# Kernel tuning notes

Hardware: AMD Instinct MI355X
Metric: run time of the kernel (lower is better)

The kernel has to match this reference:

```python
import jax, jax.numpy as jnp
import numpy as np

B, J, D, K = 2048, 15, 9, 20
HID, NF = 256, 24


def _linear_params(key, fin, fout):
    kw, kb = jax.random.split(key)
    lim = 1.0 / np.sqrt(fin)
    W = jax.random.uniform(kw, (fin, fout), minval=-lim, maxval=lim, dtype=jnp.float32)
    b = jax.random.uniform(kb, (fout,), minval=-lim, maxval=lim, dtype=jnp.float32)
    return W, b


def setup_inputs() -> dict:
    key = jax.random.key(0)
    ks = jax.random.split(key, 9)
    inp = {"dct_input": jax.random.normal(ks[0], (B, J, D, K), dtype=jnp.float32)}
    inp["q_W1"], inp["q_b1"] = _linear_params(ks[1], K, HID)
    inp["q_W2"], inp["q_b2"] = _linear_params(ks[2], HID, HID)
    inp["k_W1"], inp["k_b1"] = _linear_params(ks[3], K, HID)
    inp["k_W2"], inp["k_b2"] = _linear_params(ks[4], HID, HID)
    inp["v_W1"], inp["v_b1"] = _linear_params(ks[5], K, HID)
    inp["v_W2"], inp["v_b2"] = _linear_params(ks[6], HID, HID)
    inp["p_W1"], inp["p_b1"] = _linear_params(ks[7], 2 * HID, HID)
    inp["p_W2"], inp["p_b2"] = _linear_params(ks[8], HID, NF)
    return inp


def _mlp(x, W1, b1, W2, b2):
    return jax.nn.relu(x @ W1 + b1) @ W2 + b2


def _idct_basis(n):
    # IDCT of DCT-II with norm='ortho' (scipy.fftpack.idct default type=2):
    # x[t] = sum_k c_k * X[k] * cos(pi*k*(2t+1)/(2n)), c_0=sqrt(1/n), c_k=sqrt(2/n)
    k = jnp.arange(n, dtype=jnp.float32)[:, None]
    t = jnp.arange(n, dtype=jnp.float32)[None, :]
    c = jnp.full((n, 1), np.sqrt(2.0 / n), dtype=jnp.float32).at[0, 0].set(np.sqrt(1.0 / n))
    return c * jnp.cos(np.pi * k * (2.0 * t + 1.0) / (2.0 * n))  # [k, t]


def reference(dct_input, q_W1, q_b1, q_W2, q_b2, k_W1, k_b1, k_W2, k_b2,
              v_W1, v_b1, v_W2, v_b2, p_W1, p_b1, p_W2, p_b2):
    b, j, d, kdim = dct_input.shape
    x = dct_input.reshape(b, j * d, kdim)          # tokens = J*D
    Q = _mlp(x, q_W1, q_b1, q_W2, q_b2)            # [B, T, H]
    Kt = _mlp(x, k_W1, k_b1, k_W2, k_b2)
    V = _mlp(x, v_W1, v_b1, v_W2, v_b2)
    scores = jnp.einsum('bth,bsh->bts', Q, Kt) / np.sqrt(Q.shape[-1])
    attn = jax.nn.softmax(scores, axis=-1)
    context = jnp.einsum('bts,bsh->bth', attn, V)
    feat = jnp.concatenate([Q, context], axis=-1)  # [B, T, 2H]
    out = _mlp(feat, p_W1, p_b1, p_W2, p_b2)       # [B, T, NF] (DCT coeffs)
    out = out.reshape(b, j, d, NF).transpose(0, 3, 1, 2)  # [B, NF, J, D]
    M = _idct_basis(NF)                            # [NF(k), NF(t)]
    time = jnp.einsum('bkjd,kt->btjd', out, M)     # inverse DCT along time axis
    pred = time.reshape(b, NF, j, 3, 3)
    return pred
```

## Files before the change

### kernel.cpp

```cpp
#include <hip/hip_runtime.h>

#define BDIM 512

typedef float f32x4 __attribute__((ext_vector_type(4)));
typedef short bf16x8 __attribute__((ext_vector_type(8)));

#define MFMA(a, b, c) __builtin_amdgcn_mfma_f32_16x16x32_bf16((a), (b), (c), 0, 0, 0)

constexpr int OQ1 = 0;
constexpr int OK1w = 8192;
constexpr int OV1 = 16384;
constexpr int OQ2 = 24576;
constexpr int OK2w = 90112;
constexpr int OV2 = 155648;
constexpr int OP1 = 221184;
constexpr int OP2 = 352256;
constexpr int WTOT = 360448;

constexpr int OFF_Q   = 0;
constexpr int OFF_XS  = 73728;
constexpr int OFF_SP  = 83968;
constexpr int OFF_HT2 = 127776;
constexpr int OFF_KVT = 144160;
constexpr int OFF_RWL = 160544;
constexpr int SMEM_BYTES = 161120;

constexpr int SPS = 152;

__device__ __forceinline__ unsigned short f2b(float f) {
  unsigned int u = __float_as_uint(f);
  return (unsigned short)((u + 0x7fffu + ((u >> 16) & 1u)) >> 16);
}
__device__ __forceinline__ float bfu(unsigned short u) {
  return __uint_as_float(((unsigned int)u) << 16);
}

__device__ __forceinline__ bf16x8 frag(const unsigned short* m, int rb, int stride,
                                       int kb, int lane) {
  return *(const bf16x8*)(m + (rb + (lane & 15)) * stride + kb + ((lane >> 4) << 3));
}
__device__ __forceinline__ bf16x8 frag256s(const unsigned short* m, int rb, int kb, int lane) {
  const int row = rb + (lane & 15);
  const int c = (kb + ((lane >> 4) << 3)) ^ ((row & 7) << 3);
  return *(const bf16x8*)(m + row * 256 + c);
}
__device__ __forceinline__ bf16x8 frag32s(const unsigned short* m, int rb, int lane) {
  const int row = rb + (lane & 15);
  const int c = ((lane >> 4) << 3) ^ (((row >> 1) & 3) << 3);
  return *(const bf16x8*)(m + row * 32 + c);
}
__device__ __forceinline__ int swz256(int r, int c) { return r * 256 + (c ^ ((r & 7) << 3)); }
__device__ __forceinline__ int swz32 (int r, int c) { return r * 32  + (c ^ (((r >> 1) & 3) << 3)); }

__global__ void prep_w(const float* __restrict__ qW1, const float* __restrict__ qW2,
                       const float* __restrict__ kW1, const float* __restrict__ kW2,
                       const float* __restrict__ vW1, const float* __restrict__ vW2,
                       const float* __restrict__ pW1, const float* __restrict__ pW2,
                       unsigned short* __restrict__ ws) {
  int i = blockIdx.x * 256 + threadIdx.x;
  if (i >= WTOT) return;
  float v = 0.f;
  if (i < OQ2) {
    int sel = i >> 13, r = i & 8191;
    int o = r >> 5, k = r & 31;
    const float* W = (sel == 0) ? qW1 : (sel == 1) ? kW1 : vW1;
    if (k < 20) v = W[k * 256 + o];
  } else if (i < OP1) {
    int r = i - OQ2;
    int sel = r >> 16, q = r & 65535;
    int o = q >> 8, k = q & 255;
    const float* W = (sel == 0) ? qW2 : (sel == 1) ? kW2 : vW2;
    v = W[k * 256 + o];
  } else if (i < OP2) {
    int r = i - OP1;
    int o = r >> 9, f = r & 511;
    v = pW1[f * 256 + o];
  } else {
    int r = i - OP2;
    int o = r >> 8, k = r & 255;
    if (o < 24) v = pW2[k * 24 + o];
  }
  ws[i] = f2b(v);
}

__global__ __launch_bounds__(BDIM, 2)
void motion_mfma(const float* __restrict__ x,
                 const float* __restrict__ qb1v, const float* __restrict__ qb2v,
                 const float* __restrict__ kb1v, const float* __restrict__ kb2v,
                 const float* __restrict__ vb1v, const float* __restrict__ vb2v,
                 const float* __restrict__ pb1v, const float* __restrict__ pb2v,
                 const unsigned short* __restrict__ ws,
                 float* __restrict__ out) {
  extern __shared__ char smem[];
  unsigned short* Qs  = (unsigned short*)(smem + OFF_Q);
  unsigned short* XS  = (unsigned short*)(smem + OFF_XS);
  unsigned short* SP  = (unsigned short*)(smem + OFF_SP);
  unsigned short* Hc  = (unsigned short*)(smem + OFF_SP);
  unsigned short* HT2 = (unsigned short*)(smem + OFF_HT2);
  unsigned short* KVT = (unsigned short*)(smem + OFF_KVT);
  float* RWL = (float*)(smem + OFF_RWL);
  float* Ob  = (float*)(smem + 0);
  float* MT  = (float*)(smem + 14400);

  const int tid = threadIdx.x, lane = tid & 63, w = tid >> 6;
  const int l15 = lane & 15, rs = ((lane >> 4) << 2);
  const int cb = w * 32;
  const int b = blockIdx.x;
  const f32x4 zf4 = {0.f, 0.f, 0.f, 0.f};
  const bf16x8 zb8 = {0, 0, 0, 0, 0, 0, 0, 0};

  const float* xb = x + (size_t)b * 2700;
  for (int i = tid; i < 160 * 32; i += BDIM) {
    int r = i >> 5, c = i & 31;
    XS[swz32(r, c)] = (r < 135 && c < 20) ? f2b(xb[r * 20 + c]) : (unsigned short)0;
  }
  __syncthreads();

  {
    bf16x8 w0 = frag(ws + OQ1, cb, 32, 0, lane);
    bf16x8 w1 = frag(ws + OQ1, cb + 16, 32, 0, lane);
    float bb0 = qb1v[cb + l15], bb1 = qb1v[cb + 16 + l15];
#pragma unroll
    for (int m = 0; m < 9; ++m) {
      bf16x8 a = frag32s(XS, m * 16, lane);
      f32x4 c0 = MFMA(a, w0, zf4);
      f32x4 c1 = MFMA(a, w1, zf4);
#pragma unroll
      for (int r = 0; r < 4; ++r) {
        Hc[swz256(m * 16 + rs + r, cb + l15)]      = f2b(fmaxf(c0[r] + bb0, 0.f));
        Hc[swz256(m * 16 + rs + r, cb + 16 + l15)] = f2b(fmaxf(c1[r] + bb1, 0.f));
      }
    }
    __syncthreads();

    f32x4 acc[9][2];
#pragma unroll
    for (int m = 0; m < 9; ++m) { acc[m][0] = zf4; acc[m][1] = zf4; }
    for (int ks = 0; ks < 8; ++ks) {
      bf16x8 g0 = frag(ws + OQ2, cb, 256, ks * 32, lane);
      bf16x8 g1 = frag(ws + OQ2, cb + 16, 256, ks * 32, lane);
#pragma unroll
      for (int m = 0; m < 9; ++m) {
        bf16x8 a = frag256s(Hc, m * 16, ks * 32, lane);
        acc[m][0] = MFMA(a, g0, acc[m][0]);
        acc[m][1] = MFMA(a, g1, acc[m][1]);
      }
    }
    float bb20 = qb2v[cb + l15], bb21 = qb2v[cb + 16 + l15];
#pragma unroll
    for (int m = 0; m < 9; ++m)
#pragma unroll
      for (int r = 0; r < 4; ++r) {
        Qs[swz256(m * 16 + rs + r, cb + l15)]      = f2b(acc[m][0][r] + bb20);
        Qs[swz256(m * 16 + rs + r, cb + 16 + l15)] = f2b(acc[m][1][r] + bb21);
      }
  }
  __syncthreads();

  for (int ch = 0; ch < 5; ++ch) {
    const int s0 = ch * 32;
    {
      bf16x8 w0 = frag(ws + OK1w, cb, 32, 0, lane);
      bf16x8 w1 = frag(ws + OK1w, cb + 16, 32, 0, lane);
      float bb0 = kb1v[cb + l15], bb1 = kb1v[cb + 16 + l15];
#pragma unroll
      for (int mm = 0; mm < 2; ++mm) {
        bf16x8 a = frag32s(XS, s0 + mm * 16, lane);
        f32x4 c0 = MFMA(a, w0, zf4), c1 = MFMA(a, w1, zf4);
#pragma unroll
        for (int r = 0; r < 4; ++r) {
          HT2[swz256(mm * 16 + rs + r, cb + l15)]      = f2b(fmaxf(c0[r] + bb0, 0.f));
          HT2[swz256(mm * 16 + rs + r, cb + 16 + l15)] = f2b(fmaxf(c1[r] + bb1, 0.f));
        }
      }
    }
    __syncthreads();
    {
      f32x4 a2[2][2] = {{zf4, zf4}, {zf4, zf4}};
      for (int ks = 0; ks < 8; ++ks) {
        bf16x8 g0 = frag(ws + OK2w, cb, 256, ks * 32, lane);
        bf16x8 g1 = frag(ws + OK2w, cb + 16, 256, ks * 32, lane);
#pragma unroll
        for (int mm = 0; mm < 2; ++mm) {
          bf16x8 a = frag256s(HT2, mm * 16, ks * 32, lane);
          a2[mm][0] = MFMA(a, g0, a2[mm][0]);
          a2[mm][1] = MFMA(a, g1, a2[mm][1]);
        }
      }
      float bb0 = kb2v[cb + l15], bb1 = kb2v[cb + 16 + l15];
#pragma unroll
      for (int mm = 0; mm < 2; ++mm)
#pragma unroll
        for (int r = 0; r < 4; ++r) {
          KVT[swz256(mm * 16 + rs + r, cb + l15)]      = f2b(a2[mm][0][r] + bb0);
          KVT[swz256(mm * 16 + rs + r, cb + 16 + l15)] = f2b(a2[mm][1][r] + bb1);
        }
    }
    __syncthreads();
#pragma unroll
    for (int rep = 0; rep < 3; ++rep) {
      int j = w + rep * 8;
      if (j < 18) {
        int m = j >> 1, n = j & 1;
        int sb = s0 + n * 16;
        if (sb < 144) {
          f32x4 sa = zf4;
          for (int ks = 0; ks < 8; ++ks) {
            bf16x8 qa = frag256s(Qs, m * 16, ks * 32, lane);
            bf16x8 kf = frag256s(KVT, n * 16, ks * 32, lane);
            sa = MFMA(qa, kf, sa);
          }
#pragma unroll
          for (int r = 0; r < 4; ++r)
            SP[(m * 16 + rs + r) * SPS + sb + l15] = f2b(sa[r] * 0.0625f);
        }
      }
    }
    __syncthreads();
  }

#pragma unroll
  for (int pass = 0; pass < 2; ++pass) {
    int r = pass * 128 + (tid >> 2);
    if (r < 144) {
      int j = tid & 3;
      float mx = -1e30f;
      for (int s = j; s < 135; s += 4) mx = fmaxf(mx, bfu(SP[r * SPS + s]));
      mx = fmaxf(mx, __shfl_xor(mx, 1));
      mx = fmaxf(mx, __shfl_xor(mx, 2));
      float sum = 0.f;
      for (int s = j; s < 135; s += 4) {
        float p = __expf(bfu(SP[r * SPS + s]) - mx);
        SP[r * SPS + s] = f2b(p);
        sum += p;
      }
      sum += __shfl_xor(sum, 1);
      sum += __shfl_xor(sum, 2);
      if (j == 0) RWL[r] = sum;
      for (int s = 135 + j; s < 144; s += 4) SP[r * SPS + s] = 0;
    }
  }
  __syncthreads();

  f32x4 ctx[9][2];
#pragma unroll
  for (int m = 0; m < 9; ++m) { ctx[m][0] = zf4; ctx[m][1] = zf4; }
  for (int ch = 0; ch < 5; ++ch) {
    const int s0 = ch * 32;
    {
      bf16x8 w0 = frag(ws + OV1, cb, 32, 0, lane);
      bf16x8 w1 = frag(ws + OV1, cb + 16, 32, 0, lane);
      float bb0 = vb1v[cb + l15], bb1 = vb1v[cb + 16 + l15];
#pragma unroll
      for (int mm = 0; mm < 2; ++mm) {
        bf16x8 a = frag32s(XS, s0 + mm * 16, lane);
        f32x4 c0 = MFMA(a, w0, zf4), c1 = MFMA(a, w1, zf4);
#pragma unroll
        for (int r = 0; r < 4; ++r) {
          HT2[swz256(mm * 16 + rs + r, cb + l15)]      = f2b(fmaxf(c0[r] + bb0, 0.f));
          HT2[swz256(mm * 16 + rs + r, cb + 16 + l15)] = f2b(fmaxf(c1[r] + bb1, 0.f));
        }
      }
    }
    __syncthreads();
    {
      f32x4 a2[2][2] = {{zf4, zf4}, {zf4, zf4}};
      for (int ks = 0; ks < 8; ++ks) {
        bf16x8 g0 = frag(ws + OV2, cb, 256, ks * 32, lane);
        bf16x8 g1 = frag(ws + OV2, cb + 16, 256, ks * 32, lane);
#pragma unroll
        for (int mm = 0; mm < 2; ++mm) {
          bf16x8 a = frag256s(HT2, mm * 16, ks * 32, lane);
          a2[mm][0] = MFMA(a, g0, a2[mm][0]);
          a2[mm][1] = MFMA(a, g1, a2[mm][1]);
        }
      }
      float bb0 = vb2v[cb + l15], bb1 = vb2v[cb + 16 + l15];
#pragma unroll
      for (int mm = 0; mm < 2; ++mm)
#pragma unroll
        for (int r = 0; r < 4; ++r) {
          KVT[swz32(cb + l15,      mm * 16 + rs + r)] = f2b(a2[mm][0][r] + bb0);
          KVT[swz32(cb + 16 + l15, mm * 16 + rs + r)] = f2b(a2[mm][1][r] + bb1);
        }
    }
    __syncthreads();
    {
      bf16x8 v0 = frag32s(KVT, cb, lane);
      bf16x8 v1 = frag32s(KVT, cb + 16, lane);
      const bool mask = (ch == 4) && (lane >= 32);
#pragma unroll
      for (int m = 0; m < 9; ++m) {
        bf16x8 pa = frag(SP, m * 16, SPS, s0, lane);
        if (mask) pa = zb8;
        ctx[m][0] = MFMA(pa, v0, ctx[m][0]);
        ctx[m][1] = MFMA(pa, v1, ctx[m][1]);
      }
    }
  }
  __syncthreads();

#pragma unroll
  for (int m = 0; m < 9; ++m)
#pragma unroll
    for (int r = 0; r < 4; ++r) {
      int t = m * 16 + rs + r;
      float inv = 1.0f / RWL[t];
      Hc[swz256(t, cb + l15)]      = f2b(ctx[m][0][r] * inv);
      Hc[swz256(t, cb + 16 + l15)] = f2b(ctx[m][1][r] * inv);
    }
  __syncthreads();

  {
    float pbias0 = pb1v[cb + l15], pbias1 = pb1v[cb + 16 + l15];
    f32x4 pacc[9][2];
#pragma unroll
    for (int m = 0; m < 9; ++m) {
      pacc[m][0] = (f32x4){pbias0, pbias0, pbias0, pbias0};
      pacc[m][1] = (f32x4){pbias1, pbias1, pbias1, pbias1};
    }
    for (int ks = 0; ks < 16; ++ks) {
      bf16x8 g0 = frag(ws + OP1, cb, 512, ks * 32, lane);
      bf16x8 g1 = frag(ws + OP1, cb + 16, 512, ks * 32, lane);
      const unsigned short* As = (ks < 8) ? Qs : Hc;
      int kk = (ks & 7) * 32;
#pragma unroll
      for (int m = 0; m < 9; ++m) {
        bf16x8 a = frag256s(As, m * 16, kk, lane);
        pacc[m][0] = MFMA(a, g0, pacc[m][0]);
        pacc[m][1] = MFMA(a, g1, pacc[m][1]);
      }
    }
    __syncthreads();
#pragma unroll
    for (int m = 0; m < 9; ++m)
#pragma unroll
      for (int r = 0; r < 4; ++r) {
        Hc[swz256(m * 16 + rs + r, cb + l15)]      = f2b(fmaxf(pacc[m][0][r], 0.f));
        Hc[swz256(m * 16 + rs + r, cb + 16 + l15)] = f2b(fmaxf(pacc[m][1][r], 0.f));
      }
  }
  for (int i = tid; i < 576; i += BDIM) {
    int kk = i / 24, t = i - kk * 24;
    float c = (kk == 0) ? 0.20412414523193150f : 0.28867513459481287f;
    MT[i] = c * cosf(0.065449846949787352f * (float)(kk * (2 * t + 1)));
  }
  __syncthreads();

#pragma unroll
  for (int rep = 0; rep < 3; ++rep) {
    int j = w + rep * 8;
    if (j < 18) {
      int m = j >> 1, n = j & 1;
      f32x4 oa = zf4;
      for (int ks = 0; ks < 8; ++ks) {
        bf16x8 a = frag256s(Hc, m * 16, ks * 32, lane);
        bf16x8 g = frag(ws + OP2, n * 16, 256, ks * 32, lane);
        oa = MFMA(a, g, oa);
      }
      int c = n * 16 + l15;
      if (c < 24) {
        float bb = pb2v[c];
#pragma unroll
        for (int r = 0; r < 4; ++r)
          Ob[(m * 16 + rs + r) * 25 + c] = oa[r] + bb;
      }
    }
  }
  __syncthreads();

  for (int i = tid; i < 3240; i += BDIM) {
    int tt = i / 135, tok = i - tt * 135;
    float a = 0.f;
#pragma unroll
    for (int k = 0; k < 24; ++k)
      a = fmaf(Ob[tok * 25 + k], MT[k * 24 + tt], a);
    out[(size_t)b * 3240 + i] = a;
  }
}

extern "C" void kernel_launch(void* const* d_in, const int* in_sizes, int n_in,
                              void* d_out, int out_size, void* d_ws, size_t ws_size,
                              hipStream_t stream) {
  (void)in_sizes; (void)n_in; (void)out_size;
  if (ws_size < (size_t)WTOT * 2) return;

  const float* x   = (const float*)d_in[0];
  const float* qW1 = (const float*)d_in[1];
  const float* qb1 = (const float*)d_in[2];
  const float* qW2 = (const float*)d_in[3];
  const float* qb2 = (const float*)d_in[4];
  const float* kW1 = (const float*)d_in[5];
  const float* kb1 = (const float*)d_in[6];
  const float* kW2 = (const float*)d_in[7];
  const float* kb2 = (const float*)d_in[8];
  const float* vW1 = (const float*)d_in[9];
  const float* vb1 = (const float*)d_in[10];
  const float* vW2 = (const float*)d_in[11];
  const float* vb2 = (const float*)d_in[12];
  const float* pW1 = (const float*)d_in[13];
  const float* pb1 = (const float*)d_in[14];
  const float* pW2 = (const float*)d_in[15];
  const float* pb2 = (const float*)d_in[16];
  float* out = (float*)d_out;
  unsigned short* ws = (unsigned short*)d_ws;

  prep_w<<<dim3((WTOT + 255) / 256), dim3(256), 0, stream>>>(
      qW1, qW2, kW1, kW2, vW1, vW2, pW1, pW2, ws);

  (void)hipFuncSetAttribute((const void*)motion_mfma,
                            hipFuncAttributeMaxDynamicSharedMemorySize, SMEM_BYTES);
  motion_mfma<<<dim3(2048), dim3(BDIM), SMEM_BYTES, stream>>>(
      x, qb1, qb2, kb1, kb2, vb1, vb2, pb1, pb2, ws, out);
}
```

Baseline: 603.2 us.

## Double block size to 16 waves with one 16-column tile per wave

Raises the workgroup from 512 to 1024 threads, with each wave owning one 16-column output tile instead of two 32-column tiles. Per-wave accumulator arrays shrink by half, which lowers register pressure and aims for more waves in flight to hide MFMA and LDS latency. The softmax now runs in a single pass, and the attention-score and output-projection loops are remapped over 16 waves. Input loads and output stores are switched to nontemporal hints. The launch-bounds hint of 4 blocks of 1024 threads per CU is unlikely to be reachable given the large shared-memory footprint, and the larger block adds barrier cost.

```diff
diff --git a/kernel.cpp b/kernel.cpp
--- a/kernel.cpp
+++ b/kernel.cpp
@@ -1,6 +1,6 @@
 #include <hip/hip_runtime.h>
 
-#define BDIM 512
+#define BDIM 1024
 
 typedef float f32x4 __attribute__((ext_vector_type(4)));
 typedef short bf16x8 __attribute__((ext_vector_type(8)));
@@ -83,7 +83,7 @@
   ws[i] = f2b(v);
 }
 
-__global__ __launch_bounds__(BDIM, 2)
+__global__ __launch_bounds__(BDIM, 4)
 void motion_mfma(const float* __restrict__ x,
                  const float* __restrict__ qb1v, const float* __restrict__ qb2v,
                  const float* __restrict__ kb1v, const float* __restrict__ kb2v,
@@ -104,7 +104,7 @@
 
   const int tid = threadIdx.x, lane = tid & 63, w = tid >> 6;
   const int l15 = lane & 15, rs = ((lane >> 4) << 2);
-  const int cb = w * 32;
+  const int cb = w * 16;
   const int b = blockIdx.x;
   const f32x4 zf4 = {0.f, 0.f, 0.f, 0.f};
   const bf16x8 zb8 = {0, 0, 0, 0, 0, 0, 0, 0};
@@ -112,48 +112,41 @@
   const float* xb = x + (size_t)b * 2700;
   for (int i = tid; i < 160 * 32; i += BDIM) {
     int r = i >> 5, c = i & 31;
-    XS[swz32(r, c)] = (r < 135 && c < 20) ? f2b(xb[r * 20 + c]) : (unsigned short)0;
+    float v = (r < 135 && c < 20) ? __builtin_nontemporal_load(xb + r * 20 + c) : 0.f;
+    XS[swz32(r, c)] = f2b(v);
   }
   __syncthreads();
 
   {
     bf16x8 w0 = frag(ws + OQ1, cb, 32, 0, lane);
-    bf16x8 w1 = frag(ws + OQ1, cb + 16, 32, 0, lane);
-    float bb0 = qb1v[cb + l15], bb1 = qb1v[cb + 16 + l15];
+    float bb0 = qb1v[cb + l15];
 #pragma unroll
     for (int m = 0; m < 9; ++m) {
       bf16x8 a = frag32s(XS, m * 16, lane);
       f32x4 c0 = MFMA(a, w0, zf4);
-      f32x4 c1 = MFMA(a, w1, zf4);
-#pragma unroll
-      for (int r = 0; r < 4; ++r) {
-        Hc[swz256(m * 16 + rs + r, cb + l15)]      = f2b(fmaxf(c0[r] + bb0, 0.f));
-        Hc[swz256(m * 16 + rs + r, cb + 16 + l15)] = f2b(fmaxf(c1[r] + bb1, 0.f));
-      }
-    }
-    __syncthreads();
-
-    f32x4 acc[9][2];
-#pragma unroll
-    for (int m = 0; m < 9; ++m) { acc[m][0] = zf4; acc[m][1] = zf4; }
+#pragma unroll
+      for (int r = 0; r < 4; ++r)
+        Hc[swz256(m * 16 + rs + r, cb + l15)] = f2b(fmaxf(c0[r] + bb0, 0.f));
+    }
+    __syncthreads();
+
+    f32x4 acc[9];
+#pragma unroll
+    for (int m = 0; m < 9; ++m) acc[m] = zf4;
     for (int ks = 0; ks < 8; ++ks) {
       bf16x8 g0 = frag(ws + OQ2, cb, 256, ks * 32, lane);
-      bf16x8 g1 = frag(ws + OQ2, cb + 16, 256, ks * 32, lane);
 #pragma unroll
       for (int m = 0; m < 9; ++m) {
         bf16x8 a = frag256s(Hc, m * 16, ks * 32, lane);
-        acc[m][0] = MFMA(a, g0, acc[m][0]);
-        acc[m][1] = MFMA(a, g1, acc[m][1]);
-      }
-    }
-    float bb20 = qb2v[cb + l15], bb21 = qb2v[cb + 16 + l15];
+        acc[m] = MFMA(a, g0, acc[m]);
+      }
+    }
+    float bb20 = qb2v[cb + l15];
 #pragma unroll
     for (int m = 0; m < 9; ++m)
 #pragma unroll
-      for (int r = 0; r < 4; ++r) {
-        Qs[swz256(m * 16 + rs + r, cb + l15)]      = f2b(acc[m][0][r] + bb20);
-        Qs[swz256(m * 16 + rs + r, cb + 16 + l15)] = f2b(acc[m][1][r] + bb21);
-      }
+      for (int r = 0; r < 4; ++r)
+        Qs[swz256(m * 16 + rs + r, cb + l15)] = f2b(acc[m][r] + bb20);
   }
   __syncthreads();
 
@@ -161,67 +154,57 @@
     const int s0 = ch * 32;
     {
       bf16x8 w0 = frag(ws + OK1w, cb, 32, 0, lane);
-      bf16x8 w1 = frag(ws + OK1w, cb + 16, 32, 0, lane);
-      float bb0 = kb1v[cb + l15], bb1 = kb1v[cb + 16 + l15];
+      float bb0 = kb1v[cb + l15];
 #pragma unroll
       for (int mm = 0; mm < 2; ++mm) {
         bf16x8 a = frag32s(XS, s0 + mm * 16, lane);
-        f32x4 c0 = MFMA(a, w0, zf4), c1 = MFMA(a, w1, zf4);
-#pragma unroll
-        for (int r = 0; r < 4; ++r) {
-          HT2[swz256(mm * 16 + rs + r, cb + l15)]      = f2b(fmaxf(c0[r] + bb0, 0.f));
-          HT2[swz256(mm * 16 + rs + r, cb + 16 + l15)] = f2b(fmaxf(c1[r] + bb1, 0.f));
-        }
-      }
-    }
-    __syncthreads();
-    {
-      f32x4 a2[2][2] = {{zf4, zf4}, {zf4, zf4}};
+        f32x4 c0 = MFMA(a, w0, zf4);
+#pragma unroll
+        for (int r = 0; r < 4; ++r)
+          HT2[swz256(mm * 16 + rs + r, cb + l15)] = f2b(fmaxf(c0[r] + bb0, 0.f));
+      }
+    }
+    __syncthreads();
+    {
+      f32x4 a2[2] = {zf4, zf4};
       for (int ks = 0; ks < 8; ++ks) {
         bf16x8 g0 = frag(ws + OK2w, cb, 256, ks * 32, lane);
-        bf16x8 g1 = frag(ws + OK2w, cb + 16, 256, ks * 32, lane);
 #pragma unroll
         for (int mm = 0; mm < 2; ++mm) {
           bf16x8 a = frag256s(HT2, mm * 16, ks * 32, lane);
-          a2[mm][0] = MFMA(a, g0, a2[mm][0]);
-          a2[mm][1] = MFMA(a, g1, a2[mm][1]);
+          a2[mm] = MFMA(a, g0, a2[mm]);
         }
       }
-      float bb0 = kb2v[cb + l15], bb1 = kb2v[cb + 16 + l15];
+      float bb0 = kb2v[cb + l15];
 #pragma unroll
       for (int mm = 0; mm < 2; ++mm)
 #pragma unroll
-        for (int r = 0; r < 4; ++r) {
-          KVT[swz256(mm * 16 + rs + r, cb + l15)]      = f2b(a2[mm][0][r] + bb0);
-          KVT[swz256(mm * 16 + rs + r, cb + 16 + l15)] = f2b(a2[mm][1][r] + bb1);
-        }
-    }
-    __syncthreads();
-#pragma unroll
-    for (int rep = 0; rep < 3; ++rep) {
-      int j = w + rep * 8;
+        for (int r = 0; r < 4; ++r)
+          KVT[swz256(mm * 16 + rs + r, cb + l15)] = f2b(a2[mm][r] + bb0);
+    }
+    __syncthreads();
+#pragma unroll
+    for (int rep = 0; rep < 2; ++rep) {
+      int j = w + rep * 16;
       if (j < 18) {
         int m = j >> 1, n = j & 1;
         int sb = s0 + n * 16;
-        if (sb < 144) {
-          f32x4 sa = zf4;
-          for (int ks = 0; ks < 8; ++ks) {
-            bf16x8 qa = frag256s(Qs, m * 16, ks * 32, lane);
-            bf16x8 kf = frag256s(KVT, n * 16, ks * 32, lane);
-            sa = MFMA(qa, kf, sa);
-          }
-#pragma unroll
-          for (int r = 0; r < 4; ++r)
-            SP[(m * 16 + rs + r) * SPS + sb + l15] = f2b(sa[r] * 0.0625f);
+        f32x4 sa = zf4;
+        for (int ks = 0; ks < 8; ++ks) {
+          bf16x8 qa = frag256s(Qs, m * 16, ks * 32, lane);
+          bf16x8 kf = frag256s(KVT, n * 16, ks * 32, lane);
+          sa = MFMA(qa, kf, sa);
         }
-      }
-    }
-    __syncthreads();
-  }
-
-#pragma unroll
-  for (int pass = 0; pass < 2; ++pass) {
-    int r = pass * 128 + (tid >> 2);
+#pragma unroll
+        for (int r = 0; r < 4; ++r)
+          SP[(m * 16 + rs + r) * SPS + sb + l15] = f2b(sa[r] * 0.0625f);
+      }
+    }
+    __syncthreads();
+  }
+
+  {
+    int r = tid >> 2;
     if (r < 144) {
       int j = tid & 3;
       float mx = -1e30f;
@@ -242,59 +225,50 @@
   }
   __syncthreads();
 
-  f32x4 ctx[9][2];
-#pragma unroll
-  for (int m = 0; m < 9; ++m) { ctx[m][0] = zf4; ctx[m][1] = zf4; }
+  f32x4 ctx[9];
+#pragma unroll
+  for (int m = 0; m < 9; ++m) ctx[m] = zf4;
   for (int ch = 0; ch < 5; ++ch) {
     const int s0 = ch * 32;
     {
       bf16x8 w0 = frag(ws + OV1, cb, 32, 0, lane);
-      bf16x8 w1 = frag(ws + OV1, cb + 16, 32, 0, lane);
-      float bb0 = vb1v[cb + l15], bb1 = vb1v[cb + 16 + l15];
+      float bb0 = vb1v[cb + l15];
 #pragma unroll
       for (int mm = 0; mm < 2; ++mm) {
         bf16x8 a = frag32s(XS, s0 + mm * 16, lane);
-        f32x4 c0 = MFMA(a, w0, zf4), c1 = MFMA(a, w1, zf4);
-#pragma unroll
-        for (int r = 0; r < 4; ++r) {
-          HT2[swz256(mm * 16 + rs + r, cb + l15)]      = f2b(fmaxf(c0[r] + bb0, 0.f));
-          HT2[swz256(mm * 16 + rs + r, cb + 16 + l15)] = f2b(fmaxf(c1[r] + bb1, 0.f));
-        }
-      }
-    }
-    __syncthreads();
-    {
-      f32x4 a2[2][2] = {{zf4, zf4}, {zf4, zf4}};
+        f32x4 c0 = MFMA(a, w0, zf4);
+#pragma unroll
+        for (int r = 0; r < 4; ++r)
+          HT2[swz256(mm * 16 + rs + r, cb + l15)] = f2b(fmaxf(c0[r] + bb0, 0.f));
+      }
+    }
+    __syncthreads();
+    {
+      f32x4 a2[2] = {zf4, zf4};
       for (int ks = 0; ks < 8; ++ks) {
         bf16x8 g0 = frag(ws + OV2, cb, 256, ks * 32, lane);
-        bf16x8 g1 = frag(ws + OV2, cb + 16, 256, ks * 32, lane);
 #pragma unroll
         for (int mm = 0; mm < 2; ++mm) {
           bf16x8 a = frag256s(HT2, mm * 16, ks * 32, lane);
-          a2[mm][0] = MFMA(a, g0, a2[mm][0]);
-          a2[mm][1] = MFMA(a, g1, a2[mm][1]);
+          a2[mm] = MFMA(a, g0, a2[mm]);
         }
       }
-      float bb0 = vb2v[cb + l15], bb1 = vb2v[cb + 16 + l15];
+      float bb0 = vb2v[cb + l15];
 #pragma unroll
       for (int mm = 0; mm < 2; ++mm)
 #pragma unroll
-        for (int r = 0; r < 4; ++r) {
-          KVT[swz32(cb + l15,      mm * 16 + rs + r)] = f2b(a2[mm][0][r] + bb0);
-          KVT[swz32(cb + 16 + l15, mm * 16 + rs + r)] = f2b(a2[mm][1][r] + bb1);
-        }
+        for (int r = 0; r < 4; ++r)
+          KVT[swz32(cb + l15, mm * 16 + rs + r)] = f2b(a2[mm][r] + bb0);
     }
     __syncthreads();
     {
       bf16x8 v0 = frag32s(KVT, cb, lane);
-      bf16x8 v1 = frag32s(KVT, cb + 16, lane);
       const bool mask = (ch == 4) && (lane >= 32);
 #pragma unroll
       for (int m = 0; m < 9; ++m) {
         bf16x8 pa = frag(SP, m * 16, SPS, s0, lane);
         if (mask) pa = zb8;
-        ctx[m][0] = MFMA(pa, v0, ctx[m][0]);
-        ctx[m][1] = MFMA(pa, v1, ctx[m][1]);
+        ctx[m] = MFMA(pa, v0, ctx[m]);
       }
     }
   }
@@ -306,39 +280,37 @@
     for (int r = 0; r < 4; ++r) {
       int t = m * 16 + rs + r;
       float inv = 1.0f / RWL[t];
-      Hc[swz256(t, cb + l15)]      = f2b(ctx[m][0][r] * inv);
-      Hc[swz256(t, cb + 16 + l15)] = f2b(ctx[m][1][r] * inv);
+      Hc[swz256(t, cb + l15)] = f2b(ctx[m][r] * inv);
     }
   __syncthreads();
 
   {
-    float pbias0 = pb1v[cb + l15], pbias1 = pb1v[cb + 16 + l15];
-    f32x4 pacc[9][2];
-#pragma unroll
-    for (int m = 0; m < 9; ++m) {
-      pacc[m][0] = (f32x4){pbias0, pbias0, pbias0, pbias0};
-      pacc[m][1] = (f32x4){pbias1, pbias1, pbias1, pbias1};
-    }
-    for (int ks = 0; ks < 16; ++ks) {
+    float bbe = pb1v[cb + l15];
+    f32x4 pacc[9];
+#pragma unroll
+    for (int m = 0; m < 9; ++m) pacc[m] = (f32x4){bbe, bbe, bbe, bbe};
+    for (int ks = 0; ks < 8; ++ks) {
       bf16x8 g0 = frag(ws + OP1, cb, 512, ks * 32, lane);
-      bf16x8 g1 = frag(ws + OP1, cb + 16, 512, ks * 32, lane);
-      const unsigned short* As = (ks < 8) ? Qs : Hc;
-      int kk = (ks & 7) * 32;
 #pragma unroll
       for (int m = 0; m < 9; ++m) {
-        bf16x8 a = frag256s(As, m * 16, kk, lane);
-        pacc[m][0] = MFMA(a, g0, pacc[m][0]);
-        pacc[m][1] = MFMA(a, g1, pacc[m][1]);
+        bf16x8 a = frag256s(Qs, m * 16, ks * 32, lane);
+        pacc[m] = MFMA(a, g0, pacc[m]);
+      }
+    }
+    for (int ks = 0; ks < 8; ++ks) {
+      bf16x8 g0 = frag(ws + OP1, cb, 512, 256 + ks * 32, lane);
+#pragma unroll
+      for (int m = 0; m < 9; ++m) {
+        bf16x8 a = frag256s(Hc, m * 16, ks * 32, lane);
+        pacc[m] = MFMA(a, g0, pacc[m]);
       }
     }
     __syncthreads();
 #pragma unroll
     for (int m = 0; m < 9; ++m)
 #pragma unroll
-      for (int r = 0; r < 4; ++r) {
-        Hc[swz256(m * 16 + rs + r, cb + l15)]      = f2b(fmaxf(pacc[m][0][r], 0.f));
-        Hc[swz256(m * 16 + rs + r, cb + 16 + l15)] = f2b(fmaxf(pacc[m][1][r], 0.f));
-      }
+      for (int r = 0; r < 4; ++r)
+        Hc[swz256(m * 16 + rs + r, cb + l15)] = f2b(fmaxf(pacc[m][r], 0.f));
   }
   for (int i = tid; i < 576; i += BDIM) {
     int kk = i / 24, t = i - kk * 24;
@@ -348,8 +320,8 @@
   __syncthreads();
 
 #pragma unroll
-  for (int rep = 0; rep < 3; ++rep) {
-    int j = w + rep * 8;
+  for (int rep = 0; rep < 2; ++rep) {
+    int j = w + rep * 16;
     if (j < 18) {
       int m = j >> 1, n = j & 1;
       f32x4 oa = zf4;
@@ -375,7 +347,7 @@
 #pragma unroll
     for (int k = 0; k < 24; ++k)
       a = fmaf(Ob[tok * 25 + k], MT[k * 24 + tt], a);
-    out[(size_t)b * 3240 + i] = a;
+    __builtin_nontemporal_store(a, out + (size_t)b * 3240 + i);
   }
 }
 
```

Result: slower. 715.1 us (+18.5%).

## Software-pipeline K/V first-layer MLP with attention and unroll MFMA loops

Applied to the files above, without the earlier changes.

Hoists the K and V first-layer weight fragments and biases out of the chunk loops, then restructures both chunk loops so the next chunk's first-layer MLP into HT2 runs in the same barrier interval as the current chunk's score or context MFMAs. This removes one __syncthreads per chunk. It also fully unrolls the K-reduction loops, splits the projection loop into separate Q and context halves to drop the per-iteration pointer select, and switches input loads and output stores to nontemporal. The cost is more live registers from the hoisted fragments and the unrolling, which could reduce occupancy or cause spills.

```diff
diff --git a/kernel.cpp b/kernel.cpp
--- a/kernel.cpp
+++ b/kernel.cpp
@@ -112,9 +112,30 @@
   const float* xb = x + (size_t)b * 2700;
   for (int i = tid; i < 160 * 32; i += BDIM) {
     int r = i >> 5, c = i & 31;
-    XS[swz32(r, c)] = (r < 135 && c < 20) ? f2b(xb[r * 20 + c]) : (unsigned short)0;
-  }
-  __syncthreads();
+    float v = (r < 135 && c < 20) ? __builtin_nontemporal_load(xb + r * 20 + c) : 0.f;
+    XS[swz32(r, c)] = f2b(v);
+  }
+
+  const bf16x8 kw0 = frag(ws + OK1w, cb, 32, 0, lane);
+  const bf16x8 kw1 = frag(ws + OK1w, cb + 16, 32, 0, lane);
+  const bf16x8 vw0 = frag(ws + OV1, cb, 32, 0, lane);
+  const bf16x8 vw1 = frag(ws + OV1, cb + 16, 32, 0, lane);
+  const float kbb0 = kb1v[cb + l15], kbb1 = kb1v[cb + 16 + l15];
+  const float vbb0 = vb1v[cb + l15], vbb1 = vb1v[cb + 16 + l15];
+  __syncthreads();
+
+  auto L1 = [&](const bf16x8& u0, const bf16x8& u1, float bb0, float bb1, int s0) {
+#pragma unroll
+    for (int mm = 0; mm < 2; ++mm) {
+      bf16x8 a = frag32s(XS, s0 + mm * 16, lane);
+      f32x4 c0 = MFMA(a, u0, zf4), c1 = MFMA(a, u1, zf4);
+#pragma unroll
+      for (int r = 0; r < 4; ++r) {
+        HT2[swz256(mm * 16 + rs + r, cb + l15)]      = f2b(fmaxf(c0[r] + bb0, 0.f));
+        HT2[swz256(mm * 16 + rs + r, cb + 16 + l15)] = f2b(fmaxf(c1[r] + bb1, 0.f));
+      }
+    }
+  };
 
   {
     bf16x8 w0 = frag(ws + OQ1, cb, 32, 0, lane);
@@ -131,11 +152,14 @@
         Hc[swz256(m * 16 + rs + r, cb + 16 + l15)] = f2b(fmaxf(c1[r] + bb1, 0.f));
       }
     }
-    __syncthreads();
-
+  }
+  __syncthreads();
+
+  {
     f32x4 acc[9][2];
 #pragma unroll
     for (int m = 0; m < 9; ++m) { acc[m][0] = zf4; acc[m][1] = zf4; }
+#pragma unroll
     for (int ks = 0; ks < 8; ++ks) {
       bf16x8 g0 = frag(ws + OQ2, cb, 256, ks * 32, lane);
       bf16x8 g1 = frag(ws + OQ2, cb + 16, 256, ks * 32, lane);
@@ -157,26 +181,14 @@
   }
   __syncthreads();
 
+  L1(kw0, kw1, kbb0, kbb1, 0);
+  __syncthreads();
+
   for (int ch = 0; ch < 5; ++ch) {
     const int s0 = ch * 32;
     {
-      bf16x8 w0 = frag(ws + OK1w, cb, 32, 0, lane);
-      bf16x8 w1 = frag(ws + OK1w, cb + 16, 32, 0, lane);
-      float bb0 = kb1v[cb + l15], bb1 = kb1v[cb + 16 + l15];
-#pragma unroll
-      for (int mm = 0; mm < 2; ++mm) {
-        bf16x8 a = frag32s(XS, s0 + mm * 16, lane);
-        f32x4 c0 = MFMA(a, w0, zf4), c1 = MFMA(a, w1, zf4);
-#pragma unroll
-        for (int r = 0; r < 4; ++r) {
-          HT2[swz256(mm * 16 + rs + r, cb + l15)]      = f2b(fmaxf(c0[r] + bb0, 0.f));
-          HT2[swz256(mm * 16 + rs + r, cb + 16 + l15)] = f2b(fmaxf(c1[r] + bb1, 0.f));
-        }
-      }
-    }
-    __syncthreads();
-    {
       f32x4 a2[2][2] = {{zf4, zf4}, {zf4, zf4}};
+#pragma unroll
       for (int ks = 0; ks < 8; ++ks) {
         bf16x8 g0 = frag(ws + OK2w, cb, 256, ks * 32, lane);
         bf16x8 g1 = frag(ws + OK2w, cb + 16, 256, ks * 32, lane);
@@ -197,6 +209,8 @@
         }
     }
     __syncthreads();
+    if (ch < 4) L1(kw0, kw1, kbb0, kbb1, s0 + 32);
+    else        L1(vw0, vw1, vbb0, vbb1, 0);
 #pragma unroll
     for (int rep = 0; rep < 3; ++rep) {
       int j = w + rep * 8;
@@ -205,6 +219,7 @@
         int sb = s0 + n * 16;
         if (sb < 144) {
           f32x4 sa = zf4;
+#pragma unroll
           for (int ks = 0; ks < 8; ++ks) {
             bf16x8 qa = frag256s(Qs, m * 16, ks * 32, lane);
             bf16x8 kf = frag256s(KVT, n * 16, ks * 32, lane);
@@ -248,23 +263,8 @@
   for (int ch = 0; ch < 5; ++ch) {
     const int s0 = ch * 32;
     {
-      bf16x8 w0 = frag(ws + OV1, cb, 32, 0, lane);
-      bf16x8 w1 = frag(ws + OV1, cb + 16, 32, 0, lane);
-      float bb0 = vb1v[cb + l15], bb1 = vb1v[cb + 16 + l15];
-#pragma unroll
-      for (int mm = 0; mm < 2; ++mm) {
-        bf16x8 a = frag32s(XS, s0 + mm * 16, lane);
-        f32x4 c0 = MFMA(a, w0, zf4), c1 = MFMA(a, w1, zf4);
-#pragma unroll
-        for (int r = 0; r < 4; ++r) {
-          HT2[swz256(mm * 16 + rs + r, cb + l15)]      = f2b(fmaxf(c0[r] + bb0, 0.f));
-          HT2[swz256(mm * 16 + rs + r, cb + 16 + l15)] = f2b(fmaxf(c1[r] + bb1, 0.f));
-        }
-      }
-    }
-    __syncthreads();
-    {
       f32x4 a2[2][2] = {{zf4, zf4}, {zf4, zf4}};
+#pragma unroll
       for (int ks = 0; ks < 8; ++ks) {
         bf16x8 g0 = frag(ws + OV2, cb, 256, ks * 32, lane);
         bf16x8 g1 = frag(ws + OV2, cb + 16, 256, ks * 32, lane);
@@ -285,6 +285,7 @@
         }
     }
     __syncthreads();
+    if (ch < 4) L1(vw0, vw1, vbb0, vbb1, s0 + 32);
     {
       bf16x8 v0 = frag32s(KVT, cb, lane);
       bf16x8 v1 = frag32s(KVT, cb + 16, lane);
@@ -297,8 +298,8 @@
         ctx[m][1] = MFMA(pa, v1, ctx[m][1]);
       }
     }
-  }
-  __syncthreads();
+    __syncthreads();
+  }
 
 #pragma unroll
   for (int m = 0; m < 9; ++m)
@@ -319,14 +320,24 @@
       pacc[m][0] = (f32x4){pbias0, pbias0, pbias0, pbias0};
       pacc[m][1] = (f32x4){pbias1, pbias1, pbias1, pbias1};
     }
-    for (int ks = 0; ks < 16; ++ks) {
+#pragma unroll
+    for (int ks = 0; ks < 8; ++ks) {
       bf16x8 g0 = frag(ws + OP1, cb, 512, ks * 32, lane);
       bf16x8 g1 = frag(ws + OP1, cb + 16, 512, ks * 32, lane);
-      const unsigned short* As = (ks < 8) ? Qs : Hc;
-      int kk = (ks & 7) * 32;
 #pragma unroll
       for (int m = 0; m < 9; ++m) {
-        bf16x8 a = frag256s(As, m * 16, kk, lane);
+        bf16x8 a = frag256s(Qs, m * 16, ks * 32, lane);
+        pacc[m][0] = MFMA(a, g0, pacc[m][0]);
+        pacc[m][1] = MFMA(a, g1, pacc[m][1]);
+      }
+    }
+#pragma unroll
+    for (int ks = 0; ks < 8; ++ks) {
+      bf16x8 g0 = frag(ws + OP1, cb, 512, 256 + ks * 32, lane);
+      bf16x8 g1 = frag(ws + OP1, cb + 16, 512, 256 + ks * 32, lane);
+#pragma unroll
+      for (int m = 0; m < 9; ++m) {
+        bf16x8 a = frag256s(Hc, m * 16, ks * 32, lane);
         pacc[m][0] = MFMA(a, g0, pacc[m][0]);
         pacc[m][1] = MFMA(a, g1, pacc[m][1]);
       }
@@ -353,6 +364,7 @@
     if (j < 18) {
       int m = j >> 1, n = j & 1;
       f32x4 oa = zf4;
+#pragma unroll
       for (int ks = 0; ks < 8; ++ks) {
         bf16x8 a = frag256s(Hc, m * 16, ks * 32, lane);
         bf16x8 g = frag(ws + OP2, n * 16, 256, ks * 32, lane);
@@ -375,7 +387,7 @@
 #pragma unroll
     for (int k = 0; k < 24; ++k)
       a = fmaf(Ob[tok * 25 + k], MT[k * 24 + tt], a);
-    out[(size_t)b * 3240 + i] = a;
+    __builtin_nontemporal_store(a, out + (size_t)b * 3240 + i);
   }
 }
 
```

Result: slower. 623.8 us (+3.4%).
